# Kernel tuning notes

Measured on AMD Instinct MI355X. Metric: run time of the kernel, lower is better.

The kernel has to match this reference:

```python
import jax, jax.numpy as jnp
import numpy as np

B, T, I, H, SEQLEN = 16384, 60, 32, 128, 30


def setup_inputs() -> dict:
    key = jax.random.key(0)
    ks = jax.random.split(key, 8)
    s_ih = 1.0 / np.sqrt(H)
    return {
        "x": jax.random.normal(ks[0], (B, T, I), dtype=jnp.float32),
        "h": jax.random.normal(ks[1], (1, B, H), dtype=jnp.float32),
        # GRU params (PyTorch layout: gates [r, z, n] stacked along dim 0)
        "W_ih": jax.random.uniform(ks[2], (3 * H, I), minval=-s_ih, maxval=s_ih, dtype=jnp.float32),
        "W_hh": jax.random.uniform(ks[3], (3 * H, H), minval=-s_ih, maxval=s_ih, dtype=jnp.float32),
        "b_ih": jax.random.uniform(ks[4], (3 * H,), minval=-s_ih, maxval=s_ih, dtype=jnp.float32),
        "b_hh": jax.random.uniform(ks[5], (3 * H,), minval=-s_ih, maxval=s_ih, dtype=jnp.float32),
        # output projection: hidden -> n_inputs
        "W_out": jax.random.uniform(ks[6], (I, H), minval=-s_ih, maxval=s_ih, dtype=jnp.float32),
        "b_out": jax.random.uniform(ks[7], (I,), minval=-s_ih, maxval=s_ih, dtype=jnp.float32),
    }


def _gru_cell(x_t, h, W_ih, W_hh, b_ih, b_hh):
    # x_t: [B, I], h: [B, H]
    gi = x_t @ W_ih.T + b_ih          # [B, 3H]
    gh = h @ W_hh.T + b_hh            # [B, 3H]
    i_r, i_z, i_n = jnp.split(gi, 3, axis=-1)
    h_r, h_z, h_n = jnp.split(gh, 3, axis=-1)
    r = jax.nn.sigmoid(i_r + h_r)
    z = jax.nn.sigmoid(i_z + h_z)
    n = jnp.tanh(i_n + r * h_n)
    return (1.0 - z) * n + z * h


def reference(x, h, W_ih, W_hh, b_ih, b_hh, W_out, b_out):
    xout = x[:, SEQLEN:, :]            # [B, steps, I]
    steps = xout.shape[1]
    h0 = h[0]                          # single layer, unidirectional -> [B, H]
    x0 = xout[:, 0, :]                 # [B, I]

    def step(carry, _):
        x_t, h_t = carry
        h_new = _gru_cell(x_t, h_t, W_ih, W_hh, b_ih, b_hh)
        y = h_new @ W_out.T + b_out    # [B, I], fed back as next input
        return (y, h_new), y

    _, ys = jax.lax.scan(step, (x0, h0), None, length=steps)  # ys: [steps, B, I]
    return jnp.transpose(ys, (1, 0, 2))                        # [B, steps, I]
```

## Files before the change

### kernel.cpp

```cpp
#include <hip/hip_runtime.h>


#define NB    16384
#define TT    60
#define II    32
#define HH    128
#define NSTEP 30
#define SEQ0  30
#define BM    64
#define HBS   144
#define XBS   40

typedef __attribute__((ext_vector_type(8))) short bf16x8;
typedef __attribute__((ext_vector_type(4))) float f32x4;

#define MFMA(a, b, c) __builtin_amdgcn_mfma_f32_16x16x32_bf16((a), (b), (c), 0, 0, 0)

__device__ __forceinline__ short f2bf(float x) {
    unsigned u = __float_as_uint(x);
    u += 0x7FFFu + ((u >> 16) & 1u);
    return (short)(u >> 16);
}
__device__ __forceinline__ bf16x8 ldw8(const float* p) {
    float4 a = *(const float4*)p;
    float4 b = *(const float4*)(p + 4);
    bf16x8 f;
    f[0] = f2bf(a.x); f[1] = f2bf(a.y); f[2] = f2bf(a.z); f[3] = f2bf(a.w);
    f[4] = f2bf(b.x); f[5] = f2bf(b.y); f[6] = f2bf(b.z); f[7] = f2bf(b.w);
    return f;
}
__device__ __forceinline__ float sigm(float a)  { return 1.0f / (1.0f + __expf(-a)); }
__device__ __forceinline__ float tanhf_(float a){ return 1.0f - 2.0f / (1.0f + __expf(2.0f * a)); }

__global__ __launch_bounds__(512, 2)
void gru_mfma_kernel(const float* __restrict__ x,
                     const float* __restrict__ h0,
                     const float* __restrict__ Wih,
                     const float* __restrict__ Whh,
                     const float* __restrict__ bih,
                     const float* __restrict__ bhh,
                     const float* __restrict__ Wout,
                     const float* __restrict__ bout,
                     float* __restrict__ out)
{
    __shared__ short shb[2][BM * HBS];
    __shared__ short sxb[BM * XBS];

    const int tid    = threadIdx.x;
    const int lane   = tid & 63;
    const int wave   = __builtin_amdgcn_readfirstlane(tid >> 6);
    const int n16    = lane & 15;
    const int quad   = lane >> 4;
    const int rowblk = blockIdx.x * BM;

    bf16x8 Br[5], Bz[5], Bnh[4], Bnx;
    float  b_r, b_z, b_nh, b_nx;
    {
        const int j = wave * 16 + n16;
        const float* wr = Whh + (size_t)j * HH;
        const float* wz = Whh + (size_t)(HH + j) * HH;
        const float* wn = Whh + (size_t)(2 * HH + j) * HH;
        #pragma unroll
        for (int kt = 0; kt < 4; ++kt) {
            Br[kt]  = ldw8(wr + kt * 32 + quad * 8);
            Bz[kt]  = ldw8(wz + kt * 32 + quad * 8);
            Bnh[kt] = ldw8(wn + kt * 32 + quad * 8);
        }
        Br[4] = ldw8(Wih + (size_t)j * II + quad * 8);
        Bz[4] = ldw8(Wih + (size_t)(HH + j) * II + quad * 8);
        Bnx   = ldw8(Wih + (size_t)(2 * HH + j) * II + quad * 8);
        b_r  = bih[j] + bhh[j];
        b_z  = bih[HH + j] + bhh[HH + j];
        b_nh = bhh[2 * HH + j];
        b_nx = bih[2 * HH + j];
    }
    const int rowtile = wave >> 1;
    const int coltile = wave & 1;
    bf16x8 Bo[4];
    float  b_o;
    {
        const int i = coltile * 16 + n16;
        #pragma unroll
        for (int kt = 0; kt < 4; ++kt)
            Bo[kt] = ldw8(Wout + (size_t)i * HH + kt * 32 + quad * 8);
        b_o = bout[i];
    }

    float hst[4][4];
    {
        const int col = wave * 16 + n16;
        #pragma unroll
        for (int mt = 0; mt < 4; ++mt)
            #pragma unroll
            for (int reg = 0; reg < 4; ++reg)
                hst[mt][reg] = h0[(size_t)(rowblk + mt * 16 + quad * 4 + reg) * HH + col];
    }

    {
        const int r  = tid >> 3;
        const int c0 = (tid & 7) * 16;
        const float* src = h0 + (size_t)(rowblk + r) * HH + c0;
        *(bf16x8*)&shb[0][r * HBS + c0]     = ldw8(src);
        *(bf16x8*)&shb[0][r * HBS + c0 + 8] = ldw8(src + 8);
    }
    if (tid < 256) {
        const int r  = tid >> 2;
        const int c0 = (tid & 3) * 8;
        const float* src = x + ((size_t)(rowblk + r) * TT + SEQ0) * II + c0;
        *(bf16x8*)&sxb[r * XBS + c0] = ldw8(src);
    }
    __syncthreads();

    int p = 0;
    for (int s = 0; s < NSTEP; ++s) {
        #pragma unroll
        for (int mt = 0; mt < 4; ++mt) {
            bf16x8 A[5];
            #pragma unroll
            for (int kt = 0; kt < 4; ++kt)
                A[kt] = *(const bf16x8*)&shb[p][(mt * 16 + n16) * HBS + kt * 32 + quad * 8];
            A[4] = *(const bf16x8*)&sxb[(mt * 16 + n16) * XBS + quad * 8];

            f32x4 ar  = (f32x4){b_r,  b_r,  b_r,  b_r};
            f32x4 az  = (f32x4){b_z,  b_z,  b_z,  b_z};
            f32x4 anh = (f32x4){b_nh, b_nh, b_nh, b_nh};
            f32x4 anx = (f32x4){b_nx, b_nx, b_nx, b_nx};
            #pragma unroll
            for (int kt = 0; kt < 4; ++kt) {
                ar  = MFMA(A[kt], Br[kt],  ar);
                az  = MFMA(A[kt], Bz[kt],  az);
                anh = MFMA(A[kt], Bnh[kt], anh);
            }
            ar  = MFMA(A[4], Br[4], ar);
            az  = MFMA(A[4], Bz[4], az);
            anx = MFMA(A[4], Bnx,   anx);

            {
                const int colw = wave * 16 + n16;
                #pragma unroll
                for (int reg = 0; reg < 4; ++reg) {
                    const float r = sigm(ar[reg]);
                    const float z = sigm(az[reg]);
                    const float n = tanhf_(anx[reg] + r * anh[reg]);
                    const float hnew = n + z * (hst[mt][reg] - n);
                    hst[mt][reg] = hnew;
                    shb[1 - p][(mt * 16 + quad * 4 + reg) * HBS + colw] = f2bf(hnew);
                }
            }
        }
        __syncthreads();

        {
            bf16x8 A2[4];
            #pragma unroll
            for (int kt = 0; kt < 4; ++kt)
                A2[kt] = *(const bf16x8*)&shb[1 - p][(rowtile * 16 + n16) * HBS + kt * 32 + quad * 8];
            f32x4 yo = (f32x4){b_o, b_o, b_o, b_o};
            #pragma unroll
            for (int kt = 0; kt < 4; ++kt)
                yo = MFMA(A2[kt], Bo[kt], yo);
            #pragma unroll
            for (int reg = 0; reg < 4; ++reg) {
                const int r_l = rowtile * 16 + quad * 4 + reg;
                const float yv = yo[reg];
                out[(size_t)(rowblk + r_l) * (NSTEP * II) + s * II + coltile * 16 + n16] = yv;
                sxb[r_l * XBS + coltile * 16 + n16] = f2bf(yv);
            }
        }
        p ^= 1;
        __syncthreads();
    }
}

extern "C" void kernel_launch(void* const* d_in, const int* in_sizes, int n_in,
                              void* d_out, int out_size, void* d_ws, size_t ws_size,
                              hipStream_t stream) {
    (void)in_sizes; (void)n_in; (void)out_size; (void)d_ws; (void)ws_size;
    const float* x    = (const float*)d_in[0];
    const float* h0   = (const float*)d_in[1];
    const float* Wih  = (const float*)d_in[2];
    const float* Whh  = (const float*)d_in[3];
    const float* bih  = (const float*)d_in[4];
    const float* bhh  = (const float*)d_in[5];
    const float* Wout = (const float*)d_in[6];
    const float* bout = (const float*)d_in[7];
    float* out = (float*)d_out;

    dim3 grid(NB / BM);
    dim3 block(512);
    gru_mfma_kernel<<<grid, block, 0, stream>>>(x, h0, Wih, Whh, bih, bhh,
                                                Wout, bout, out);
}
```

Baseline: 313.3 us.

## Fold output projection into input weights to remove the per-step x path

A small pre-kernel precomputes W_ih·W_out and the matching folded biases into the workspace. After the first step, the recurrence then reads only h: the r and z gates use Whh+Wih·Wout, and the n gate gets a separate input-side term from h. This removes the sxb round trip and one barrier per step, and the MFMA stages are reordered so each step computes its output projection first. It also shrinks the LDS row stride, uses hardware rcp in the activations, and adds a second kernel launch and extra register pressure for the folded weights.

After: 268.5 us. 1.17x faster.

```diff
diff --git a/kernel.cpp b/kernel.cpp
--- a/kernel.cpp
+++ b/kernel.cpp
@@ -8,8 +8,11 @@
 #define NSTEP 30
 #define SEQ0  30
 #define BM    64
-#define HBS   144
+#define HBS   136
 #define XBS   40
+
+#define WS_WSTAR 0
+#define WS_BSTAR (384 * 128)
 
 typedef __attribute__((ext_vector_type(8))) short bf16x8;
 typedef __attribute__((ext_vector_type(4))) float f32x4;
@@ -29,8 +32,36 @@
     f[4] = f2bf(b.x); f[5] = f2bf(b.y); f[6] = f2bf(b.z); f[7] = f2bf(b.w);
     return f;
 }
-__device__ __forceinline__ float sigm(float a)  { return 1.0f / (1.0f + __expf(-a)); }
-__device__ __forceinline__ float tanhf_(float a){ return 1.0f - 2.0f / (1.0f + __expf(2.0f * a)); }
+__device__ __forceinline__ float sigm(float a) {
+    return __builtin_amdgcn_rcpf(1.0f + __expf(-a));
+}
+__device__ __forceinline__ float tanh_(float a) {
+    return 1.0f - 2.0f * __builtin_amdgcn_rcpf(1.0f + __expf(2.0f * a));
+}
+
+__global__ void fold_kernel(const float* __restrict__ Wih,
+                            const float* __restrict__ Whh,
+                            const float* __restrict__ bih,
+                            const float* __restrict__ bhh,
+                            const float* __restrict__ Wout,
+                            const float* __restrict__ bout,
+                            float* __restrict__ ws)
+{
+    const int jg = blockIdx.x;
+    const int k  = threadIdx.x;
+    const int gate = jg >> 7;
+    float acc  = (gate < 2) ? Whh[(size_t)jg * HH + k] : 0.0f;
+    float bacc = 0.0f;
+    #pragma unroll 8
+    for (int i = 0; i < II; ++i) {
+        const float w = Wih[(size_t)jg * II + i];
+        acc  += w * Wout[(size_t)i * HH + k];
+        bacc += w * bout[i];
+    }
+    ws[WS_WSTAR + (size_t)jg * HH + k] = acc;
+    if (k == 0)
+        ws[WS_BSTAR + jg] = bih[jg] + ((gate < 2) ? bhh[jg] : 0.0f) + bacc;
+}
 
 __global__ __launch_bounds__(512, 2)
 void gru_mfma_kernel(const float* __restrict__ x,
@@ -41,6 +72,7 @@
                      const float* __restrict__ bhh,
                      const float* __restrict__ Wout,
                      const float* __restrict__ bout,
+                     const float* __restrict__ ws,
                      float* __restrict__ out)
 {
     __shared__ short shb[2][BM * HBS];
@@ -52,27 +84,16 @@
     const int n16    = lane & 15;
     const int quad   = lane >> 4;
     const int rowblk = blockIdx.x * BM;
-
-    bf16x8 Br[5], Bz[5], Bnh[4], Bnx;
-    float  b_r, b_z, b_nh, b_nx;
-    {
-        const int j = wave * 16 + n16;
-        const float* wr = Whh + (size_t)j * HH;
-        const float* wz = Whh + (size_t)(HH + j) * HH;
+    const int j      = wave * 16 + n16;
+
+    bf16x8 Bnh[4];
+    float  b_nh;
+    {
         const float* wn = Whh + (size_t)(2 * HH + j) * HH;
         #pragma unroll
-        for (int kt = 0; kt < 4; ++kt) {
-            Br[kt]  = ldw8(wr + kt * 32 + quad * 8);
-            Bz[kt]  = ldw8(wz + kt * 32 + quad * 8);
+        for (int kt = 0; kt < 4; ++kt)
             Bnh[kt] = ldw8(wn + kt * 32 + quad * 8);
-        }
-        Br[4] = ldw8(Wih + (size_t)j * II + quad * 8);
-        Bz[4] = ldw8(Wih + (size_t)(HH + j) * II + quad * 8);
-        Bnx   = ldw8(Wih + (size_t)(2 * HH + j) * II + quad * 8);
-        b_r  = bih[j] + bhh[j];
-        b_z  = bih[HH + j] + bhh[HH + j];
         b_nh = bhh[2 * HH + j];
-        b_nx = bih[2 * HH + j];
     }
     const int rowtile = wave >> 1;
     const int coltile = wave & 1;
@@ -87,14 +108,11 @@
     }
 
     float hst[4][4];
-    {
-        const int col = wave * 16 + n16;
-        #pragma unroll
-        for (int mt = 0; mt < 4; ++mt)
-            #pragma unroll
-            for (int reg = 0; reg < 4; ++reg)
-                hst[mt][reg] = h0[(size_t)(rowblk + mt * 16 + quad * 4 + reg) * HH + col];
-    }
+    #pragma unroll
+    for (int mt = 0; mt < 4; ++mt)
+        #pragma unroll
+        for (int reg = 0; reg < 4; ++reg)
+            hst[mt][reg] = h0[(size_t)(rowblk + mt * 16 + quad * 4 + reg) * HH + j];
 
     {
         const int r  = tid >> 3;
@@ -111,50 +129,84 @@
     }
     __syncthreads();
 
+    {
+        bf16x8 Br0[4], Bz0[4], Bxr, Bxz, Bxn;
+        const float* wr = Whh + (size_t)j * HH;
+        const float* wz = Whh + (size_t)(HH + j) * HH;
+        #pragma unroll
+        for (int kt = 0; kt < 4; ++kt) {
+            Br0[kt] = ldw8(wr + kt * 32 + quad * 8);
+            Bz0[kt] = ldw8(wz + kt * 32 + quad * 8);
+        }
+        Bxr = ldw8(Wih + (size_t)j * II + quad * 8);
+        Bxz = ldw8(Wih + (size_t)(HH + j) * II + quad * 8);
+        Bxn = ldw8(Wih + (size_t)(2 * HH + j) * II + quad * 8);
+        const float b_r0 = bih[j] + bhh[j];
+        const float b_z0 = bih[HH + j] + bhh[HH + j];
+        const float b_n0 = bih[2 * HH + j];
+
+        #pragma unroll
+        for (int mt = 0; mt < 4; ++mt) {
+            bf16x8 A[4], Ax;
+            #pragma unroll
+            for (int kt = 0; kt < 4; ++kt)
+                A[kt] = *(const bf16x8*)&shb[0][(mt * 16 + n16) * HBS + kt * 32 + quad * 8];
+            Ax = *(const bf16x8*)&sxb[(mt * 16 + n16) * XBS + quad * 8];
+
+            f32x4 ar  = (f32x4){b_r0, b_r0, b_r0, b_r0};
+            f32x4 az  = (f32x4){b_z0, b_z0, b_z0, b_z0};
+            f32x4 anh = (f32x4){b_nh, b_nh, b_nh, b_nh};
+            f32x4 anx = (f32x4){b_n0, b_n0, b_n0, b_n0};
+            #pragma unroll
+            for (int kt = 0; kt < 4; ++kt) {
+                ar  = MFMA(A[kt], Br0[kt], ar);
+                az  = MFMA(A[kt], Bz0[kt], az);
+                anh = MFMA(A[kt], Bnh[kt], anh);
+            }
+            ar  = MFMA(Ax, Bxr, ar);
+            az  = MFMA(Ax, Bxz, az);
+            anx = MFMA(Ax, Bxn, anx);
+
+            #pragma unroll
+            for (int reg = 0; reg < 4; ++reg) {
+                const float r = sigm(ar[reg]);
+                const float z = sigm(az[reg]);
+                const float n = tanh_(anx[reg] + r * anh[reg]);
+                const float hnew = n + z * (hst[mt][reg] - n);
+                hst[mt][reg] = hnew;
+                shb[1][(mt * 16 + quad * 4 + reg) * HBS + j] = f2bf(hnew);
+            }
+        }
+    }
+
+    bf16x8 Brs[4], Bzs[4], Bni[4];
+    float  b_rs, b_zs, b_ni;
+    {
+        const float* pr = ws + WS_WSTAR + (size_t)j * HH;
+        const float* pz = ws + WS_WSTAR + (size_t)(HH + j) * HH;
+        const float* pn = ws + WS_WSTAR + (size_t)(2 * HH + j) * HH;
+        #pragma unroll
+        for (int kt = 0; kt < 4; ++kt) {
+            Brs[kt] = ldw8(pr + kt * 32 + quad * 8);
+            Bzs[kt] = ldw8(pz + kt * 32 + quad * 8);
+            Bni[kt] = ldw8(pn + kt * 32 + quad * 8);
+        }
+        b_rs = ws[WS_BSTAR + j];
+        b_zs = ws[WS_BSTAR + HH + j];
+        b_ni = ws[WS_BSTAR + 2 * HH + j];
+    }
+
+    __syncthreads();
+
     int p = 0;
     for (int s = 0; s < NSTEP; ++s) {
-        #pragma unroll
-        for (int mt = 0; mt < 4; ++mt) {
-            bf16x8 A[5];
-            #pragma unroll
-            for (int kt = 0; kt < 4; ++kt)
-                A[kt] = *(const bf16x8*)&shb[p][(mt * 16 + n16) * HBS + kt * 32 + quad * 8];
-            A[4] = *(const bf16x8*)&sxb[(mt * 16 + n16) * XBS + quad * 8];
-
-            f32x4 ar  = (f32x4){b_r,  b_r,  b_r,  b_r};
-            f32x4 az  = (f32x4){b_z,  b_z,  b_z,  b_z};
-            f32x4 anh = (f32x4){b_nh, b_nh, b_nh, b_nh};
-            f32x4 anx = (f32x4){b_nx, b_nx, b_nx, b_nx};
-            #pragma unroll
-            for (int kt = 0; kt < 4; ++kt) {
-                ar  = MFMA(A[kt], Br[kt],  ar);
-                az  = MFMA(A[kt], Bz[kt],  az);
-                anh = MFMA(A[kt], Bnh[kt], anh);
-            }
-            ar  = MFMA(A[4], Br[4], ar);
-            az  = MFMA(A[4], Bz[4], az);
-            anx = MFMA(A[4], Bnx,   anx);
-
-            {
-                const int colw = wave * 16 + n16;
-                #pragma unroll
-                for (int reg = 0; reg < 4; ++reg) {
-                    const float r = sigm(ar[reg]);
-                    const float z = sigm(az[reg]);
-                    const float n = tanhf_(anx[reg] + r * anh[reg]);
-                    const float hnew = n + z * (hst[mt][reg] - n);
-                    hst[mt][reg] = hnew;
-                    shb[1 - p][(mt * 16 + quad * 4 + reg) * HBS + colw] = f2bf(hnew);
-                }
-            }
-        }
-        __syncthreads();
+        const int q = 1 - p;
 
         {
             bf16x8 A2[4];
             #pragma unroll
             for (int kt = 0; kt < 4; ++kt)
-                A2[kt] = *(const bf16x8*)&shb[1 - p][(rowtile * 16 + n16) * HBS + kt * 32 + quad * 8];
+                A2[kt] = *(const bf16x8*)&shb[q][(rowtile * 16 + n16) * HBS + kt * 32 + quad * 8];
             f32x4 yo = (f32x4){b_o, b_o, b_o, b_o};
             #pragma unroll
             for (int kt = 0; kt < 4; ++kt)
@@ -162,12 +214,43 @@
             #pragma unroll
             for (int reg = 0; reg < 4; ++reg) {
                 const int r_l = rowtile * 16 + quad * 4 + reg;
-                const float yv = yo[reg];
-                out[(size_t)(rowblk + r_l) * (NSTEP * II) + s * II + coltile * 16 + n16] = yv;
-                sxb[r_l * XBS + coltile * 16 + n16] = f2bf(yv);
-            }
-        }
-        p ^= 1;
+                out[(size_t)(rowblk + r_l) * (NSTEP * II) + s * II + coltile * 16 + n16] = yo[reg];
+            }
+        }
+
+        if (s == NSTEP - 1) break;
+
+        #pragma unroll
+        for (int mt = 0; mt < 4; ++mt) {
+            bf16x8 A[4];
+            #pragma unroll
+            for (int kt = 0; kt < 4; ++kt)
+                A[kt] = *(const bf16x8*)&shb[q][(mt * 16 + n16) * HBS + kt * 32 + quad * 8];
+
+            f32x4 ar  = (f32x4){b_rs, b_rs, b_rs, b_rs};
+            f32x4 az  = (f32x4){b_zs, b_zs, b_zs, b_zs};
+            f32x4 anh = (f32x4){b_nh, b_nh, b_nh, b_nh};
+            f32x4 ani = (f32x4){b_ni, b_ni, b_ni, b_ni};
+            #pragma unroll
+            for (int kt = 0; kt < 4; ++kt) {
+                ar  = MFMA(A[kt], Brs[kt], ar);
+                az  = MFMA(A[kt], Bzs[kt], az);
+                anh = MFMA(A[kt], Bnh[kt], anh);
+                ani = MFMA(A[kt], Bni[kt], ani);
+            }
+
+            #pragma unroll
+            for (int reg = 0; reg < 4; ++reg) {
+                const float r = sigm(ar[reg]);
+                const float z = sigm(az[reg]);
+                const float n = tanh_(ani[reg] + r * anh[reg]);
+                const float hnew = n + z * (hst[mt][reg] - n);
+                hst[mt][reg] = hnew;
+                shb[p][(mt * 16 + quad * 4 + reg) * HBS + j] = f2bf(hnew);
+            }
+        }
+
+        p = q;
         __syncthreads();
     }
 }
@@ -175,7 +258,7 @@
 extern "C" void kernel_launch(void* const* d_in, const int* in_sizes, int n_in,
                               void* d_out, int out_size, void* d_ws, size_t ws_size,
                               hipStream_t stream) {
-    (void)in_sizes; (void)n_in; (void)out_size; (void)d_ws; (void)ws_size;
+    (void)in_sizes; (void)n_in; (void)out_size; (void)ws_size;
     const float* x    = (const float*)d_in[0];
     const float* h0   = (const float*)d_in[1];
     const float* Wih  = (const float*)d_in[2];
@@ -185,9 +268,12 @@
     const float* Wout = (const float*)d_in[6];
     const float* bout = (const float*)d_in[7];
     float* out = (float*)d_out;
-
+    float* ws  = (float*)d_ws;
+
+    fold_kernel<<<dim3(384), dim3(128), 0, stream>>>(Wih, Whh, bih, bhh,
+                                                     Wout, bout, ws);
     dim3 grid(NB / BM);
     dim3 block(512);
     gru_mfma_kernel<<<grid, block, 0, stream>>>(x, h0, Wih, Whh, bih, bhh,
-                                                Wout, bout, out);
-}
+                                                Wout, bout, ws, out);
+}
```
